# Kernel optimization log

Hardware: AMD Instinct MI355X
Metric: run time of the kernel (lower is better)

The kernel has to match this reference:

```python
import jax, jax.numpy as jnp
import numpy as np

N_NODES = 10000
N_EDGES = 160000
IN_C, HID_C, OUT_C = 256, 512, 256
DROP_P = 0.5


def setup_inputs() -> dict:
    key = jax.random.key(0)
    ks = jax.random.split(key, 6)
    tensor = jax.random.normal(ks[0], (N_NODES, IN_C), dtype=jnp.float32)
    edge_index = jax.random.randint(ks[1], (2, N_EDGES), 0, N_NODES, dtype=jnp.int64)
    # Glorot-ish init for GCNConv linear weights, zero bias (PyG default bias init is zeros)
    W1 = jax.random.normal(ks[2], (IN_C, HID_C), dtype=jnp.float32) * (1.0 / np.sqrt(IN_C))
    b1 = jnp.zeros((HID_C,), dtype=jnp.float32)
    W2 = jax.random.normal(ks[3], (HID_C, OUT_C), dtype=jnp.float32) * (1.0 / np.sqrt(HID_C))
    b2 = jnp.zeros((OUT_C,), dtype=jnp.float32)
    return {"tensor": tensor, "edge_index": edge_index, "W1": W1, "b1": b1, "W2": W2, "b2": b2}


def _gcn_layer(x, W, b, src, dst, n_nodes):
    # x' = D^{-1/2} (A + I) D^{-1/2} X W + b  (PyG GCNConv, add_self_loops=True)
    xw = x @ W                                             # [N, C_out]
    deg = jax.ops.segment_sum(jnp.ones(src.shape[0], xw.dtype), dst,
                              num_segments=n_nodes)        # includes self-loops -> deg >= 1
    dinv = jax.lax.rsqrt(deg)
    norm = dinv[src] * dinv[dst]                           # [E+N]
    msg = xw[src] * norm[:, None]                          # gather + normalize
    out = jax.ops.segment_sum(msg, dst, num_segments=n_nodes)  # scatter-add
    return out + b


def _dropout(x, key, p):
    keep = jax.random.bernoulli(key, 1.0 - p, x.shape)
    return jnp.where(keep, x / (1.0 - p), jnp.zeros((), x.dtype))


def reference(tensor, edge_index, W1, b1, W2, b2):
    n = tensor.shape[0]
    src, dst = edge_index[0], edge_index[1]
    loops = jnp.arange(n, dtype=src.dtype)
    src_f = jnp.concatenate([src, loops])
    dst_f = jnp.concatenate([dst, loops])

    dk1, dk2 = jax.random.split(jax.random.key(42))
    h = _gcn_layer(tensor, W1, b1, src_f, dst_f, n)
    h = jax.nn.relu(h)
    h = _dropout(h, dk1, DROP_P)
    h = _gcn_layer(h, W2, b2, src_f, dst_f, n)
    h = jax.nn.relu(h)
    h = _dropout(h, dk2, DROP_P)
    return h
```

## Files before the change

### kernel.cpp

```cpp
#include <hip/hip_runtime.h>
#include <stdint.h>


#define C_IN 256
#define C_HID 512
#define C_OUT 256

typedef unsigned short ushort_t;
typedef __bf16 bf16x8 __attribute__((ext_vector_type(8)));
typedef float floatx4 __attribute__((ext_vector_type(4)));

typedef __attribute__((address_space(1))) const void g1_void;
typedef __attribute__((address_space(3))) void l3_void;

__device__ __forceinline__ void gll16(const ushort_t* g, ushort_t* l) {
  __builtin_amdgcn_global_load_lds((g1_void*)g, (l3_void*)l, 16, 0, 0);
}

__host__ __device__ __forceinline__ void tf_rounds(unsigned& x0, unsigned& x1,
                                                   unsigned k0, unsigned k1) {
  unsigned k2 = k0 ^ k1 ^ 0x1BD11BDAu;
#define ROT(r) { x0 += x1; x1 = (x1 << r) | (x1 >> (32 - r)); x1 ^= x0; }
  x0 += k0; x1 += k1;
  ROT(13) ROT(15) ROT(26) ROT(6)
  x0 += k1; x1 += k2 + 1u;
  ROT(17) ROT(29) ROT(16) ROT(24)
  x0 += k2; x1 += k0 + 2u;
  ROT(13) ROT(15) ROT(26) ROT(6)
  x0 += k0; x1 += k1 + 3u;
  ROT(17) ROT(29) ROT(16) ROT(24)
  x0 += k1; x1 += k2 + 4u;
  ROT(13) ROT(15) ROT(26) ROT(6)
  x0 += k2; x1 += k0 + 5u;
#undef ROT
}

__device__ __forceinline__ float drop_scale(unsigned j, unsigned k0, unsigned k1) {
  unsigned x0 = 0u, x1 = j;
  tf_rounds(x0, x1, k0, k1);
  unsigned bits = x0 ^ x1;
  float u = __uint_as_float((bits >> 9) | 0x3f800000u) - 1.0f;
  return (u < 0.5f) ? 2.0f : 0.0f;
}

__device__ __forceinline__ ushort_t f2bf(float f) {
  unsigned u = __float_as_uint(f);
  unsigned r = (u + 0x7fffu + ((u >> 16) & 1u)) >> 16;
  return (ushort_t)r;
}
__device__ __forceinline__ float bf2f(ushort_t h) {
  return __uint_as_float(((unsigned)h) << 16);
}

__global__ __launch_bounds__(256) void k_setup(const unsigned* __restrict__ raw,
                                               unsigned* __restrict__ flag,
                                               int* __restrict__ cnt, int N, int NB,
                                               const float* __restrict__ W1,
                                               const float* __restrict__ W2,
                                               ushort_t* __restrict__ h1,
                                               ushort_t* __restrict__ l1,
                                               ushort_t* __restrict__ h2,
                                               ushort_t* __restrict__ l2) {
  int b = blockIdx.x, t = threadIdx.x;
  if (b < NB) {
    int i = b * 256 + t;
    if (i < N) cnt[i] = 0;
    return;
  }
  if (b == NB) {
    __shared__ unsigned sh[256];
    unsigned acc = 0;
    for (int i = 1 + 2 * t; i < 8192; i += 512) acc |= raw[i];
    sh[t] = acc;
    __syncthreads();
    for (int s = 128; s > 0; s >>= 1) {
      if (t < s) sh[t] |= sh[t + s];
      __syncthreads();
    }
    if (t == 0) *flag = (sh[0] == 0u) ? 1u : 0u;
    return;
  }
  int idx = (b - NB - 1) * 256 + t;
  const int S1 = C_IN * C_HID;
  if (idx >= S1 + C_HID * C_OUT) return;
  const float* W; ushort_t *hi, *lo; int K, Nn, li;
  if (idx < S1) { W = W1; hi = h1; lo = l1; K = C_IN; Nn = C_HID; li = idx; }
  else { W = W2; hi = h2; lo = l2; K = C_HID; Nn = C_OUT; li = idx - S1; }
  int k = li / Nn, n = li - k * Nn;
  float v = W[li];
  ushort_t h = f2bf(v);
  hi[(size_t)n * K + k] = h;
  lo[(size_t)n * K + k] = f2bf(v - bf2f(h));
}

__global__ __launch_bounds__(256) void k_convert(const void* __restrict__ raw,
                                                 const unsigned* __restrict__ flag,
                                                 int* __restrict__ eic,
                                                 int* __restrict__ cnt,
                                                 int E) {
  int i = blockIdx.x * 256 + threadIdx.x;
  if (i >= 2 * E) return;
  int v;
  if (*flag) v = (int)((const long long*)raw)[i];
  else       v = ((const int*)raw)[i];
  eic[i] = v;
  if (i >= E) atomicAdd(&cnt[v], 1);
}

__global__ __launch_bounds__(256) void k_scan_a(const int* __restrict__ cnt,
                                                int* __restrict__ bsum, int n) {
  __shared__ int sh[256];
  int i = blockIdx.x * 256 + threadIdx.x;
  sh[threadIdx.x] = (i < n) ? cnt[i] : 0;
  __syncthreads();
  for (int s = 128; s > 0; s >>= 1) {
    if ((int)threadIdx.x < s) sh[threadIdx.x] += sh[threadIdx.x + s];
    __syncthreads();
  }
  if (threadIdx.x == 0) bsum[blockIdx.x] = sh[0];
}

__global__ __launch_bounds__(256) void k_scan_c(const int* __restrict__ cnt,
                                                const int* __restrict__ bsum,
                                                int* __restrict__ roff,
                                                int* __restrict__ cursor,
                                                float* __restrict__ dinv,
                                                int n, int NB, int E) {
  __shared__ int sh[256];
  __shared__ int spre;
  int t = threadIdx.x;
  if (t < 64) {
    int v = (t < (int)blockIdx.x && t < NB) ? bsum[t] : 0;
    for (int s = 32; s > 0; s >>= 1) v += __shfl_down(v, s);
    if (t == 0) spre = v;
  }
  int i = blockIdx.x * 256 + t;
  int v = (i < n) ? cnt[i] : 0;
  sh[t] = v;
  __syncthreads();
  for (int s = 1; s < 256; s <<= 1) {
    int tv = (t >= s) ? sh[t - s] : 0;
    __syncthreads();
    sh[t] += tv;
    __syncthreads();
  }
  if (i < n) {
    int excl = spre + sh[t] - v;
    roff[i] = excl;
    cursor[i] = excl;
    dinv[i] = rsqrtf((float)(v + 1));
  }
  if (blockIdx.x == 0 && t == 0) roff[n] = E;
}

__global__ __launch_bounds__(256) void k_scatter(const int* __restrict__ eic,
                                                 int* __restrict__ cursor,
                                                 int* __restrict__ csr, int E) {
  int e = blockIdx.x * 256 + threadIdx.x;
  if (e >= E) return;
  int s = eic[e], d = eic[E + e];
  int slot = atomicAdd(&cursor[d], 1);
  csr[slot] = s;
}

template <int EPI, int PRE>
__global__ __launch_bounds__(256) void k_gather4(const int* __restrict__ roff,
                                                 const int* __restrict__ csr,
                                                 const float* __restrict__ dinv,
                                                 const float* __restrict__ x,
                                                 const float* __restrict__ bias,
                                                 void* __restrict__ o1,
                                                 void* __restrict__ o2,
                                                 unsigned dk0, unsigned dk1) {
  int g = threadIdx.x >> 6;
  int tg = threadIdx.x & 63;
  int node = blockIdx.x * 4 + g;
  float dd = dinv[node];
  const float4* xr = (const float4*)x;
  float4 v = xr[(size_t)node * 64 + tg];
  float4 acc;
  if (PRE) acc = v;
  else acc = make_float4(dd * v.x, dd * v.y, dd * v.z, dd * v.w);
  int p = roff[node], end = roff[node + 1];
  for (; p + 8 <= end; p += 8) {
    int s[8];
#pragma unroll
    for (int q = 0; q < 8; ++q) s[q] = csr[p + q];
    float4 r[8];
#pragma unroll
    for (int q = 0; q < 8; ++q) r[q] = xr[(size_t)s[q] * 64 + tg];
    if (PRE) {
#pragma unroll
      for (int q = 0; q < 8; ++q) {
        acc.x += r[q].x; acc.y += r[q].y; acc.z += r[q].z; acc.w += r[q].w;
      }
    } else {
      float w[8];
#pragma unroll
      for (int q = 0; q < 8; ++q) w[q] = dinv[s[q]];
#pragma unroll
      for (int q = 0; q < 8; ++q) {
        acc.x += w[q] * r[q].x; acc.y += w[q] * r[q].y;
        acc.z += w[q] * r[q].z; acc.w += w[q] * r[q].w;
      }
    }
  }
  for (; p + 4 <= end; p += 4) {
    int s0 = csr[p], s1 = csr[p + 1], s2 = csr[p + 2], s3 = csr[p + 3];
    float4 a = xr[(size_t)s0 * 64 + tg];
    float4 b = xr[(size_t)s1 * 64 + tg];
    float4 c = xr[(size_t)s2 * 64 + tg];
    float4 d = xr[(size_t)s3 * 64 + tg];
    if (PRE) {
      acc.x += a.x + b.x + c.x + d.x;
      acc.y += a.y + b.y + c.y + d.y;
      acc.z += a.z + b.z + c.z + d.z;
      acc.w += a.w + b.w + c.w + d.w;
    } else {
      float w0 = dinv[s0], w1 = dinv[s1], w2 = dinv[s2], w3 = dinv[s3];
      acc.x += w0 * a.x + w1 * b.x + w2 * c.x + w3 * d.x;
      acc.y += w0 * a.y + w1 * b.y + w2 * c.y + w3 * d.y;
      acc.z += w0 * a.z + w1 * b.z + w2 * c.z + w3 * d.z;
      acc.w += w0 * a.w + w1 * b.w + w2 * c.w + w3 * d.w;
    }
  }
  for (; p < end; ++p) {
    int s0 = csr[p];
    float4 a = xr[(size_t)s0 * 64 + tg];
    if (PRE) {
      acc.x += a.x; acc.y += a.y; acc.z += a.z; acc.w += a.w;
    } else {
      float w0 = dinv[s0];
      acc.x += w0 * a.x; acc.y += w0 * a.y; acc.z += w0 * a.z; acc.w += w0 * a.w;
    }
  }
  acc.x *= dd; acc.y *= dd; acc.z *= dd; acc.w *= dd;
  if (EPI) {
    float4 bb = ((const float4*)bias)[tg];
    acc.x = fmaxf(acc.x + bb.x, 0.0f);
    acc.y = fmaxf(acc.y + bb.y, 0.0f);
    acc.z = fmaxf(acc.z + bb.z, 0.0f);
    acc.w = fmaxf(acc.w + bb.w, 0.0f);
    unsigned jb = (unsigned)node * 256u + (unsigned)tg * 4u;
    acc.x *= drop_scale(jb + 0u, dk0, dk1);
    acc.y *= drop_scale(jb + 1u, dk0, dk1);
    acc.z *= drop_scale(jb + 2u, dk0, dk1);
    acc.w *= drop_scale(jb + 3u, dk0, dk1);
    ((float4*)o1)[(size_t)node * 64 + tg] = acc;
  } else {
    ushort_t h0 = f2bf(acc.x), h1 = f2bf(acc.y), h2 = f2bf(acc.z), h3 = f2bf(acc.w);
    ushort4 hv = make_ushort4(h0, h1, h2, h3);
    ushort4 lv = make_ushort4(f2bf(acc.x - bf2f(h0)), f2bf(acc.y - bf2f(h1)),
                              f2bf(acc.z - bf2f(h2)), f2bf(acc.w - bf2f(h3)));
    ((ushort4*)o1)[(size_t)node * 64 + tg] = hv;
    ((ushort4*)o2)[(size_t)node * 64 + tg] = lv;
  }
}

template <int EPI>
__global__ __launch_bounds__(256) void k_gemm3(
    const ushort_t* __restrict__ Ahi, const ushort_t* __restrict__ Alo,
    const ushort_t* __restrict__ Bhi, const ushort_t* __restrict__ Blo,
    const float* __restrict__ bias, const float* __restrict__ dscale,
    ushort_t* __restrict__ Chi, ushort_t* __restrict__ Clo,
    float* __restrict__ Cf,
    int M, int N, int K, unsigned dk0, unsigned dk1) {
  __shared__ ushort_t sAh[64 * 32], sAl[64 * 32], sBh[128 * 32], sBl[128 * 32];
  const int t = threadIdx.x;
  const int lane = t & 63, wave = t >> 6;
  const int wm = wave & 1, wn = wave >> 1;
  const int quad = lane >> 4, l16 = lane & 15;
  const int row0 = blockIdx.y * 64, col0 = blockIdx.x * 128;
  const int srow = t >> 2;
  const int skc = (t & 3) * 8;

  floatx4 acc[2][4] = {};

  const int ra  = min(row0 + srow, M - 1);
  const int rb0 = col0 + srow;
  const int rb1 = col0 + 64 + srow;

  const ushort_t* gAh = Ahi + (size_t)ra * K + skc;
  const ushort_t* gAl = Alo + (size_t)ra * K + skc;
  const ushort_t* gB0h = Bhi + (size_t)rb0 * K + skc;
  const ushort_t* gB1h = Bhi + (size_t)rb1 * K + skc;
  const ushort_t* gB0l = Blo + (size_t)rb0 * K + skc;
  const ushort_t* gB1l = Blo + (size_t)rb1 * K + skc;
  ushort_t* lAh = &sAh[wave * 512];
  ushort_t* lAl = &sAl[wave * 512];
  ushort_t* lB0h = &sBh[wave * 512];
  ushort_t* lB1h = &sBh[2048 + wave * 512];
  ushort_t* lB0l = &sBl[wave * 512];
  ushort_t* lB1l = &sBl[2048 + wave * 512];

  for (int kt = 0; kt < K; kt += 32) {
    gll16(gAh + kt, lAh);
    gll16(gAl + kt, lAl);
    gll16(gB0h + kt, lB0h);
    gll16(gB1h + kt, lB1h);
    gll16(gB0l + kt, lB0l);
    gll16(gB1l + kt, lB1l);
    __syncthreads();

    bf16x8 ah[2], al[2], bh[4], bl[4];
#pragma unroll
    for (int i = 0; i < 2; ++i) {
      int off = (wm * 32 + i * 16 + l16) * 32 + quad * 8;
      ah[i] = *(const bf16x8*)&sAh[off];
      al[i] = *(const bf16x8*)&sAl[off];
    }
#pragma unroll
    for (int j = 0; j < 4; ++j) {
      int off = (wn * 64 + j * 16 + l16) * 32 + quad * 8;
      bh[j] = *(const bf16x8*)&sBh[off];
      bl[j] = *(const bf16x8*)&sBl[off];
    }
#pragma unroll
    for (int i = 0; i < 2; ++i)
#pragma unroll
      for (int j = 0; j < 4; ++j) {
        acc[i][j] = __builtin_amdgcn_mfma_f32_16x16x32_bf16(ah[i], bh[j], acc[i][j], 0, 0, 0);
        acc[i][j] = __builtin_amdgcn_mfma_f32_16x16x32_bf16(ah[i], bl[j], acc[i][j], 0, 0, 0);
        acc[i][j] = __builtin_amdgcn_mfma_f32_16x16x32_bf16(al[i], bh[j], acc[i][j], 0, 0, 0);
      }
    __syncthreads();
  }

#pragma unroll
  for (int i = 0; i < 2; ++i) {
#pragma unroll
    for (int j = 0; j < 4; ++j) {
      int gc = col0 + wn * 64 + j * 16 + l16;
#pragma unroll
      for (int reg = 0; reg < 4; ++reg) {
        int gr = row0 + wm * 32 + i * 16 + quad * 4 + reg;
        if (gr >= M) continue;
        float v = acc[i][j][reg];
        size_t o = (size_t)gr * N + gc;
        if (EPI) {
          v += bias[gc];
          v = fmaxf(v, 0.0f);
          v *= drop_scale((unsigned)gr * (unsigned)N + (unsigned)gc, dk0, dk1);
          ushort_t h = f2bf(v);
          Chi[o] = h;
          Clo[o] = f2bf(v - bf2f(h));
        } else {
          Cf[o] = v * dscale[gr];
        }
      }
    }
  }
}

extern "C" void kernel_launch(void* const* d_in, const int* in_sizes, int n_in,
                              void* d_out, int out_size, void* d_ws, size_t ws_size,
                              hipStream_t stream) {
  const float* x  = (const float*)d_in[0];
  const void*  ei = d_in[1];
  const float* W1 = (const float*)d_in[2];
  const float* b1 = (const float*)d_in[3];
  const float* W2 = (const float*)d_in[4];
  const float* b2 = (const float*)d_in[5];
  float* out = (float*)d_out;

  const int N = in_sizes[0] / C_IN;
  const int E = in_sizes[1] / 2;
  const int NB = (N + 255) / 256;

  unsigned a0 = 0u, a1 = 0u, b0 = 0u, b1k = 1u;
  tf_rounds(a0, a1, 0u, 42u);
  tf_rounds(b0, b1k, 0u, 42u);

  uintptr_t base = (uintptr_t)d_ws;
  unsigned*  flag   = (unsigned*)base;
  int*       bsum   = (int*)(base + 4096);
  int*       cnt    = (int*)(base + 16 * 1024);
  int*       roff   = (int*)(base + 64 * 1024);
  int*       cursor = (int*)(base + 128 * 1024);
  float*     dinv   = (float*)(base + 192 * 1024);
  int*       eic    = (int*)(base + 256 * 1024);
  int*       csr    = (int*)(base + 2u * 1024 * 1024);
  ushort_t*  Ahi    = (ushort_t*)(base + 4u  * 1024 * 1024);
  ushort_t*  Alo    = (ushort_t*)(base + 10u * 1024 * 1024);
  ushort_t*  H1hi   = (ushort_t*)(base + 16u * 1024 * 1024);
  ushort_t*  H1lo   = (ushort_t*)(base + 27u * 1024 * 1024);
  float*     hw2    = (float*)(base + 38u * 1024 * 1024);
  ushort_t*  W1thi  = (ushort_t*)(base + 49u * 1024 * 1024);
  ushort_t*  W1tlo  = (ushort_t*)(base + 49u * 1024 * 1024 + 512 * 1024);
  ushort_t*  W2thi  = (ushort_t*)(base + 50u * 1024 * 1024);
  ushort_t*  W2tlo  = (ushort_t*)(base + 50u * 1024 * 1024 + 512 * 1024);

  dim3 b256(256);
  const int WCB = (C_IN * C_HID + C_HID * C_OUT + 255) / 256;

  k_setup<<<dim3(NB + 1 + WCB), b256, 0, stream>>>((const unsigned*)ei, flag, cnt,
                                                   N, NB, W1, W2,
                                                   W1thi, W1tlo, W2thi, W2tlo);
  k_convert<<<dim3((2 * E + 255) / 256), b256, 0, stream>>>(ei, flag, eic, cnt, E);
  k_scan_a<<<dim3(NB), b256, 0, stream>>>(cnt, bsum, N);
  k_scan_c<<<dim3(NB), b256, 0, stream>>>(cnt, bsum, roff, cursor, dinv, N, NB, E);
  k_scatter<<<dim3((E + 255) / 256), b256, 0, stream>>>(eic, cursor, csr, E);
  k_gather4<0, 0><<<dim3(N / 4), b256, 0, stream>>>(roff, csr, dinv, x, nullptr,
                                                    Ahi, Alo, 0u, 0u);
  k_gemm3<1><<<dim3(C_HID / 128, (N + 63) / 64), b256, 0, stream>>>(
      Ahi, Alo, W1thi, W1tlo, b1, nullptr, H1hi, H1lo, nullptr,
      N, C_HID, C_IN, a0, a1);
  k_gemm3<0><<<dim3(C_OUT / 128, (N + 63) / 64), b256, 0, stream>>>(
      H1hi, H1lo, W2thi, W2tlo, nullptr, dinv, nullptr, nullptr, hw2,
      N, C_OUT, C_HID, 0u, 0u);
  k_gather4<1, 1><<<dim3(N / 4), b256, 0, stream>>>(roff, csr, dinv, hw2, b2,
                                                    out, nullptr, b0, b1k);
}
```

Measured before the change: 198.7 us.

## Fuse preprocessing into cooperative kernel and double-buffer GEMM LDS with swizzle

```diff
diff --git a/kernel.cpp b/kernel.cpp
--- a/kernel.cpp
+++ b/kernel.cpp
@@ -1,4 +1,5 @@
 #include <hip/hip_runtime.h>
+#include <hip/hip_cooperative_groups.h>
 #include <stdint.h>
 
 
@@ -12,6 +13,8 @@
 
 typedef __attribute__((address_space(1))) const void g1_void;
 typedef __attribute__((address_space(3))) void l3_void;
+
+namespace cg = cooperative_groups;
 
 __device__ __forceinline__ void gll16(const ushort_t* g, ushort_t* l) {
   __builtin_amdgcn_global_load_lds((g1_void*)g, (l3_void*)l, 16, 0, 0);
@@ -52,115 +55,120 @@
   return __uint_as_float(((unsigned)h) << 16);
 }
 
-__global__ __launch_bounds__(256) void k_setup(const unsigned* __restrict__ raw,
-                                               unsigned* __restrict__ flag,
-                                               int* __restrict__ cnt, int N, int NB,
-                                               const float* __restrict__ W1,
-                                               const float* __restrict__ W2,
-                                               ushort_t* __restrict__ h1,
-                                               ushort_t* __restrict__ l1,
-                                               ushort_t* __restrict__ h2,
-                                               ushort_t* __restrict__ l2) {
-  int b = blockIdx.x, t = threadIdx.x;
-  if (b < NB) {
-    int i = b * 256 + t;
-    if (i < N) cnt[i] = 0;
-    return;
-  }
-  if (b == NB) {
-    __shared__ unsigned sh[256];
-    unsigned acc = 0;
-    for (int i = 1 + 2 * t; i < 8192; i += 512) acc |= raw[i];
-    sh[t] = acc;
+__global__ __launch_bounds__(256) void k_pre(
+    const void* __restrict__ raw, unsigned* __restrict__ flag,
+    int* __restrict__ cnt, int* __restrict__ bsum,
+    int* __restrict__ roff, int* __restrict__ cursor,
+    float* __restrict__ dinv, int* __restrict__ eic, int* __restrict__ csr,
+    int N, int NB, int E,
+    const float* __restrict__ W1, const float* __restrict__ W2,
+    ushort_t* __restrict__ wh1, ushort_t* __restrict__ wl1,
+    ushort_t* __restrict__ wh2, ushort_t* __restrict__ wl2) {
+  cg::grid_group gg = cg::this_grid();
+  const int t = threadIdx.x;
+  __shared__ int sh[256];
+  __shared__ int spre;
+
+  const int S1 = C_IN * C_HID;
+  const int WCB = (S1 + C_HID * C_OUT + 255) / 256;
+  for (int vb = blockIdx.x; vb < NB + 1 + WCB; vb += gridDim.x) {
+    if (vb < NB) {
+      int i = vb * 256 + t;
+      if (i < N) cnt[i] = 0;
+    } else if (vb == NB) {
+      unsigned acc = 0;
+      const unsigned* r32 = (const unsigned*)raw;
+      for (int i = 1 + 2 * t; i < 8192; i += 512) acc |= r32[i];
+      ((unsigned*)sh)[t] = acc;
+      __syncthreads();
+      for (int s = 128; s > 0; s >>= 1) {
+        if (t < s) ((unsigned*)sh)[t] |= ((unsigned*)sh)[t + s];
+        __syncthreads();
+      }
+      if (t == 0) *flag = (((unsigned*)sh)[0] == 0u) ? 1u : 0u;
+    } else {
+      int idx = (vb - NB - 1) * 256 + t;
+      if (idx < S1 + C_HID * C_OUT) {
+        if (idx < S1) {
+          int k = idx >> 9, n = idx & 511;
+          float v = W1[idx];
+          ushort_t h = f2bf(v);
+          wh1[(size_t)n * C_IN + k] = h;
+          wl1[(size_t)n * C_IN + k] = f2bf(v - bf2f(h));
+        } else {
+          int li = idx - S1;
+          int k = li >> 8, n = li & 255;
+          float v = W2[li];
+          ushort_t h = f2bf(v);
+          wh2[(size_t)n * C_HID + k] = h;
+          wl2[(size_t)n * C_HID + k] = f2bf(v - bf2f(h));
+        }
+      }
+    }
+    __syncthreads();
+  }
+  gg.sync();
+
+  for (int vb = blockIdx.x; vb < (2 * E + 255) / 256; vb += gridDim.x) {
+    int i = vb * 256 + t;
+    if (i < 2 * E) {
+      int v;
+      if (*flag) v = (int)((const long long*)raw)[i];
+      else       v = ((const int*)raw)[i];
+      eic[i] = v;
+      if (i >= E) atomicAdd(&cnt[v], 1);
+    }
+  }
+  gg.sync();
+
+  for (int vb = blockIdx.x; vb < NB; vb += gridDim.x) {
+    int i = vb * 256 + t;
+    sh[t] = (i < N) ? cnt[i] : 0;
     __syncthreads();
     for (int s = 128; s > 0; s >>= 1) {
-      if (t < s) sh[t] |= sh[t + s];
+      if (t < s) sh[t] += sh[t + s];
       __syncthreads();
     }
-    if (t == 0) *flag = (sh[0] == 0u) ? 1u : 0u;
-    return;
-  }
-  int idx = (b - NB - 1) * 256 + t;
-  const int S1 = C_IN * C_HID;
-  if (idx >= S1 + C_HID * C_OUT) return;
-  const float* W; ushort_t *hi, *lo; int K, Nn, li;
-  if (idx < S1) { W = W1; hi = h1; lo = l1; K = C_IN; Nn = C_HID; li = idx; }
-  else { W = W2; hi = h2; lo = l2; K = C_HID; Nn = C_OUT; li = idx - S1; }
-  int k = li / Nn, n = li - k * Nn;
-  float v = W[li];
-  ushort_t h = f2bf(v);
-  hi[(size_t)n * K + k] = h;
-  lo[(size_t)n * K + k] = f2bf(v - bf2f(h));
-}
-
-__global__ __launch_bounds__(256) void k_convert(const void* __restrict__ raw,
-                                                 const unsigned* __restrict__ flag,
-                                                 int* __restrict__ eic,
-                                                 int* __restrict__ cnt,
-                                                 int E) {
-  int i = blockIdx.x * 256 + threadIdx.x;
-  if (i >= 2 * E) return;
-  int v;
-  if (*flag) v = (int)((const long long*)raw)[i];
-  else       v = ((const int*)raw)[i];
-  eic[i] = v;
-  if (i >= E) atomicAdd(&cnt[v], 1);
-}
-
-__global__ __launch_bounds__(256) void k_scan_a(const int* __restrict__ cnt,
-                                                int* __restrict__ bsum, int n) {
-  __shared__ int sh[256];
-  int i = blockIdx.x * 256 + threadIdx.x;
-  sh[threadIdx.x] = (i < n) ? cnt[i] : 0;
-  __syncthreads();
-  for (int s = 128; s > 0; s >>= 1) {
-    if ((int)threadIdx.x < s) sh[threadIdx.x] += sh[threadIdx.x + s];
+    if (t == 0) bsum[vb] = sh[0];
     __syncthreads();
   }
-  if (threadIdx.x == 0) bsum[blockIdx.x] = sh[0];
-}
-
-__global__ __launch_bounds__(256) void k_scan_c(const int* __restrict__ cnt,
-                                                const int* __restrict__ bsum,
-                                                int* __restrict__ roff,
-                                                int* __restrict__ cursor,
-                                                float* __restrict__ dinv,
-                                                int n, int NB, int E) {
-  __shared__ int sh[256];
-  __shared__ int spre;
-  int t = threadIdx.x;
-  if (t < 64) {
-    int v = (t < (int)blockIdx.x && t < NB) ? bsum[t] : 0;
-    for (int s = 32; s > 0; s >>= 1) v += __shfl_down(v, s);
-    if (t == 0) spre = v;
-  }
-  int i = blockIdx.x * 256 + t;
-  int v = (i < n) ? cnt[i] : 0;
-  sh[t] = v;
-  __syncthreads();
-  for (int s = 1; s < 256; s <<= 1) {
-    int tv = (t >= s) ? sh[t - s] : 0;
+  gg.sync();
+
+  for (int vb = blockIdx.x; vb < NB; vb += gridDim.x) {
+    if (t < 64) {
+      int v = (t < vb) ? bsum[t] : 0;
+      for (int s = 32; s > 0; s >>= 1) v += __shfl_down(v, s);
+      if (t == 0) spre = v;
+    }
+    int i = vb * 256 + t;
+    int v = (i < N) ? cnt[i] : 0;
+    sh[t] = v;
     __syncthreads();
-    sh[t] += tv;
+    for (int s = 1; s < 256; s <<= 1) {
+      int tv = (t >= s) ? sh[t - s] : 0;
+      __syncthreads();
+      sh[t] += tv;
+      __syncthreads();
+    }
+    if (i < N) {
+      int excl = spre + sh[t] - v;
+      roff[i] = excl;
+      cursor[i] = excl;
+      dinv[i] = rsqrtf((float)(v + 1));
+    }
+    if (vb == 0 && t == 0) roff[N] = E;
     __syncthreads();
   }
-  if (i < n) {
-    int excl = spre + sh[t] - v;
-    roff[i] = excl;
-    cursor[i] = excl;
-    dinv[i] = rsqrtf((float)(v + 1));
-  }
-  if (blockIdx.x == 0 && t == 0) roff[n] = E;
-}
-
-__global__ __launch_bounds__(256) void k_scatter(const int* __restrict__ eic,
-                                                 int* __restrict__ cursor,
-                                                 int* __restrict__ csr, int E) {
-  int e = blockIdx.x * 256 + threadIdx.x;
-  if (e >= E) return;
-  int s = eic[e], d = eic[E + e];
-  int slot = atomicAdd(&cursor[d], 1);
-  csr[slot] = s;
+  gg.sync();
+
+  for (int vb = blockIdx.x; vb < (E + 255) / 256; vb += gridDim.x) {
+    int e = vb * 256 + t;
+    if (e < E) {
+      int s = eic[e], d = eic[E + e];
+      int slot = atomicAdd(&cursor[d], 1);
+      csr[slot] = s;
+    }
+  }
 }
 
 template <int EPI, int PRE>
@@ -265,14 +273,16 @@
     ushort_t* __restrict__ Chi, ushort_t* __restrict__ Clo,
     float* __restrict__ Cf,
     int M, int N, int K, unsigned dk0, unsigned dk1) {
-  __shared__ ushort_t sAh[64 * 32], sAl[64 * 32], sBh[128 * 32], sBl[128 * 32];
+  __shared__ ushort_t sAh[2][64 * 32], sAl[2][64 * 32];
+  __shared__ ushort_t sBh[2][128 * 32], sBl[2][128 * 32];
   const int t = threadIdx.x;
   const int lane = t & 63, wave = t >> 6;
   const int wm = wave & 1, wn = wave >> 1;
   const int quad = lane >> 4, l16 = lane & 15;
   const int row0 = blockIdx.y * 64, col0 = blockIdx.x * 128;
   const int srow = t >> 2;
-  const int skc = (t & 3) * 8;
+  const int skc = (((t & 3) ^ ((t >> 3) & 3)) * 8);
+  const int qx8 = (quad ^ ((l16 >> 1) & 3)) * 8;
 
   floatx4 acc[2][4] = {};
 
@@ -286,34 +296,38 @@
   const ushort_t* gB1h = Bhi + (size_t)rb1 * K + skc;
   const ushort_t* gB0l = Blo + (size_t)rb0 * K + skc;
   const ushort_t* gB1l = Blo + (size_t)rb1 * K + skc;
-  ushort_t* lAh = &sAh[wave * 512];
-  ushort_t* lAl = &sAl[wave * 512];
-  ushort_t* lB0h = &sBh[wave * 512];
-  ushort_t* lB1h = &sBh[2048 + wave * 512];
-  ushort_t* lB0l = &sBl[wave * 512];
-  ushort_t* lB1l = &sBl[2048 + wave * 512];
-
-  for (int kt = 0; kt < K; kt += 32) {
-    gll16(gAh + kt, lAh);
-    gll16(gAl + kt, lAl);
-    gll16(gB0h + kt, lB0h);
-    gll16(gB1h + kt, lB1h);
-    gll16(gB0l + kt, lB0l);
-    gll16(gB1l + kt, lB1l);
-    __syncthreads();
+
+#define STAGE(c, kt) {                                  \
+    gll16(gAh + (kt), &sAh[c][wave * 512]);             \
+    gll16(gAl + (kt), &sAl[c][wave * 512]);             \
+    gll16(gB0h + (kt), &sBh[c][wave * 512]);            \
+    gll16(gB1h + (kt), &sBh[c][2048 + wave * 512]);     \
+    gll16(gB0l + (kt), &sBl[c][wave * 512]);            \
+    gll16(gB1l + (kt), &sBl[c][2048 + wave * 512]); }
+
+  const int nk = K >> 5;
+  STAGE(0, 0)
+  for (int it = 0; it < nk; ++it) {
+    const int c = it & 1;
+    if (it + 1 < nk) {
+      STAGE(c ^ 1, (it + 1) * 32)
+      asm volatile("s_waitcnt vmcnt(6)\n\ts_barrier" ::: "memory");
+    } else {
+      asm volatile("s_waitcnt vmcnt(0)\n\ts_barrier" ::: "memory");
+    }
 
     bf16x8 ah[2], al[2], bh[4], bl[4];
 #pragma unroll
     for (int i = 0; i < 2; ++i) {
-      int off = (wm * 32 + i * 16 + l16) * 32 + quad * 8;
-      ah[i] = *(const bf16x8*)&sAh[off];
-      al[i] = *(const bf16x8*)&sAl[off];
+      int off = (wm * 32 + i * 16 + l16) * 32 + qx8;
+      ah[i] = *(const bf16x8*)&sAh[c][off];
+      al[i] = *(const bf16x8*)&sAl[c][off];
     }
 #pragma unroll
     for (int j = 0; j < 4; ++j) {
-      int off = (wn * 64 + j * 16 + l16) * 32 + quad * 8;
-      bh[j] = *(const bf16x8*)&sBh[off];
-      bl[j] = *(const bf16x8*)&sBl[off];
+      int off = (wn * 64 + j * 16 + l16) * 32 + qx8;
+      bh[j] = *(const bf16x8*)&sBh[c][off];
+      bl[j] = *(const bf16x8*)&sBl[c][off];
     }
 #pragma unroll
     for (int i = 0; i < 2; ++i)
@@ -323,8 +337,9 @@
         acc[i][j] = __builtin_amdgcn_mfma_f32_16x16x32_bf16(ah[i], bl[j], acc[i][j], 0, 0, 0);
         acc[i][j] = __builtin_amdgcn_mfma_f32_16x16x32_bf16(al[i], bh[j], acc[i][j], 0, 0, 0);
       }
-    __syncthreads();
-  }
+    asm volatile("s_barrier" ::: "memory");
+  }
+#undef STAGE
 
 #pragma unroll
   for (int i = 0; i < 2; ++i) {
@@ -391,15 +406,17 @@
   ushort_t*  W2tlo  = (ushort_t*)(base + 50u * 1024 * 1024 + 512 * 1024);
 
   dim3 b256(256);
-  const int WCB = (C_IN * C_HID + C_HID * C_OUT + 255) / 256;
-
-  k_setup<<<dim3(NB + 1 + WCB), b256, 0, stream>>>((const unsigned*)ei, flag, cnt,
-                                                   N, NB, W1, W2,
-                                                   W1thi, W1tlo, W2thi, W2tlo);
-  k_convert<<<dim3((2 * E + 255) / 256), b256, 0, stream>>>(ei, flag, eic, cnt, E);
-  k_scan_a<<<dim3(NB), b256, 0, stream>>>(cnt, bsum, N);
-  k_scan_c<<<dim3(NB), b256, 0, stream>>>(cnt, bsum, roff, cursor, dinv, N, NB, E);
-  k_scatter<<<dim3((E + 255) / 256), b256, 0, stream>>>(eic, cursor, csr, E);
+
+  int Nv = N, NBv = NB, Ev = E;
+  const void* rawp = ei;
+  void* args[] = {
+      (void*)&rawp, (void*)&flag, (void*)&cnt, (void*)&bsum, (void*)&roff,
+      (void*)&cursor, (void*)&dinv, (void*)&eic, (void*)&csr,
+      (void*)&Nv, (void*)&NBv, (void*)&Ev,
+      (void*)&W1, (void*)&W2,
+      (void*)&W1thi, (void*)&W1tlo, (void*)&W2thi, (void*)&W2tlo};
+  hipLaunchCooperativeKernel((const void*)k_pre, dim3(1024), b256, args, 0, stream);
+
   k_gather4<0, 0><<<dim3(N / 4), b256, 0, stream>>>(roff, csr, dinv, x, nullptr,
                                                     Ahi, Alo, 0u, 0u);
   k_gemm3<1><<<dim3(C_HID / 128, (N + 63) / 64), b256, 0, stream>>>(
```

Measured after the change: 651.5 us. +227.9%, slower.
